# Kernel optimization log

Hardware: AMD Instinct MI355X
Metric: run time of the kernel (lower is better)

Reference implementation:

```python
import jax, jax.numpy as jnp
import numpy as np

E = 1024      # emb_size
H = 16        # num_heads
DH = E // H   # per-head dim (attn_output_emb_size)
DFF = 4096    # d_ff
LE = 4        # num_encoders
LD = 4        # num_decoders
B = 4
S_SRC = 512
S_TGT = 512
EPS = 1e-5
SCALE = float(np.sqrt(DH))


def _layernorm(x, g, b):
    m = jnp.mean(x, axis=-1, keepdims=True)
    v = jnp.mean((x - m) ** 2, axis=-1, keepdims=True)
    return (x - m) / jnp.sqrt(v + EPS) * g + b


def _mha(xq, xk, xv, wqkv, wo, bo, mask):
    # xq: [B,Sq,E]; wqkv: [3,H,E,DH]; mask: [B,Sq,St] or [B,1,St] with 0 / -inf entries.
    # Fuses the per-head SingleHeadSelfAttention loop into batched einsums; the
    # torch.cat(heads, dim=-1) order equals transpose(b,s,h,d)->reshape(b,s,E).
    Bn, Sq, En = xq.shape
    q = jnp.einsum('bse,hed->bhsd', xq, wqkv[0])
    k = jnp.einsum('bte,hed->bhtd', xk, wqkv[1])
    v = jnp.einsum('bte,hed->bhtd', xv, wqkv[2])
    scores = jnp.einsum('bhsd,bhtd->bhst', q, k) / SCALE
    # masked_fill(mask == -inf, -inf)
    scores = jnp.where(jnp.isneginf(mask)[:, None, :, :], -jnp.inf, scores)
    w = jax.nn.softmax(scores, axis=-1)
    o = jnp.einsum('bhst,bhtd->bhsd', w, v)
    o = o.transpose(0, 2, 1, 3).reshape(Bn, Sq, En)
    return o @ wo + bo


def _ffn(x, w1, b1, w2, b2):
    return jax.nn.relu(x @ w1 + b1) @ w2 + b2


def _forward(src, tgt, src_mask, tgt_mask, src_pad, tgt_pad, ep, dp):
    x = src.transpose(1, 0, 2)  # [B,Ss,E] (module is seq-first, heads go batch-first)
    y = tgt.transpose(1, 0, 2)  # [B,St,E]
    enc_mask = src_mask[None] + src_pad[:, None, :]   # [B,Ss,Ss]
    self_mask = tgt_mask[None] + tgt_pad[:, None, :]  # [B,St,St]
    cross_mask = src_pad[:, None, :]                  # [B,1,Ss]
    (wqkv, wo, bo, w1, b1, w2, b2, lg, lb) = ep
    for i in range(LE):  # post-norm encoder blocks
        x = x + _mha(x, x, x, wqkv[i], wo[i], bo[i], enc_mask)
        x = _layernorm(x, lg[i, 0], lb[i, 0])
        x = x + _ffn(x, w1[i], b1[i], w2[i], b2[i])
        x = _layernorm(x, lg[i, 1], lb[i, 1])
    (sqkv, swo, sbo, cqkv, cwo, cbo, dw1, db1, dw2, db2, dlg, dlb) = dp
    for i in range(LD):  # post-norm decoder blocks
        y = y + _mha(y, y, y, sqkv[i], swo[i], sbo[i], self_mask)
        y = _layernorm(y, dlg[i, 0], dlb[i, 0])
        y = y + _mha(y, x, x, cqkv[i], cwo[i], cbo[i], cross_mask)
        y = _layernorm(y, dlg[i, 1], dlb[i, 1])
        y = y + _ffn(y, dw1[i], db1[i], dw2[i], db2[i])
        y = _layernorm(y, dlg[i, 2], dlb[i, 2])
    return y.transpose(1, 0, 2)  # back to [St,B,E]


def setup_inputs() -> dict:
    key = jax.random.key(0)
    ks = iter(jax.random.split(key, 32))
    def p(shape):
        return jax.random.normal(next(ks), shape, jnp.float32) * 0.02
    # causal mask as produced by generate_square_subsequent_mask (0 on/below diag, -inf above)
    causal = jnp.where(jnp.triu(jnp.ones((S_TGT, S_TGT), bool), 1), -jnp.inf, 0.0).astype(jnp.float32)
    return {
        'src': jax.random.normal(next(ks), (S_SRC, B, E), jnp.float32),
        'tgt': jax.random.normal(next(ks), (S_TGT, B, E), jnp.float32),
        'src_mask': jnp.zeros((S_SRC, S_SRC), jnp.float32),
        'tgt_mask': causal,
        'src_padding_mask': jnp.zeros((B, S_SRC), jnp.float32),
        'tgt_padding_mask': jnp.zeros((B, S_TGT), jnp.float32),
        'enc_wqkv': p((LE, 3, H, E, DH)), 'enc_wo': p((LE, E, E)), 'enc_bo': jnp.zeros((LE, E), jnp.float32),
        'enc_ff_w1': p((LE, E, DFF)), 'enc_ff_b1': jnp.zeros((LE, DFF), jnp.float32),
        'enc_ff_w2': p((LE, DFF, E)), 'enc_ff_b2': jnp.zeros((LE, E), jnp.float32),
        'enc_ln_g': jnp.ones((LE, 2, E), jnp.float32), 'enc_ln_b': jnp.zeros((LE, 2, E), jnp.float32),
        'dec_wqkv_self': p((LD, 3, H, E, DH)), 'dec_wo_self': p((LD, E, E)), 'dec_bo_self': jnp.zeros((LD, E), jnp.float32),
        'dec_wqkv_cross': p((LD, 3, H, E, DH)), 'dec_wo_cross': p((LD, E, E)), 'dec_bo_cross': jnp.zeros((LD, E), jnp.float32),
        'dec_ff_w1': p((LD, E, DFF)), 'dec_ff_b1': jnp.zeros((LD, DFF), jnp.float32),
        'dec_ff_w2': p((LD, DFF, E)), 'dec_ff_b2': jnp.zeros((LD, E), jnp.float32),
        'dec_ln_g': jnp.ones((LD, 3, E), jnp.float32), 'dec_ln_b': jnp.zeros((LD, 3, E), jnp.float32),
    }


def reference(src, tgt, src_mask, tgt_mask, src_padding_mask, tgt_padding_mask,
              enc_wqkv, enc_wo, enc_bo, enc_ff_w1, enc_ff_b1, enc_ff_w2, enc_ff_b2,
              enc_ln_g, enc_ln_b,
              dec_wqkv_self, dec_wo_self, dec_bo_self,
              dec_wqkv_cross, dec_wo_cross, dec_bo_cross,
              dec_ff_w1, dec_ff_b1, dec_ff_w2, dec_ff_b2, dec_ln_g, dec_ln_b):
    ep = (enc_wqkv, enc_wo, enc_bo, enc_ff_w1, enc_ff_b1, enc_ff_w2, enc_ff_b2, enc_ln_g, enc_ln_b)
    dp = (dec_wqkv_self, dec_wo_self, dec_bo_self, dec_wqkv_cross, dec_wo_cross, dec_bo_cross,
          dec_ff_w1, dec_ff_b1, dec_ff_w2, dec_ff_b2, dec_ln_g, dec_ln_b)
    return _forward(src, tgt, src_mask, tgt_mask, src_padding_mask, tgt_padding_mask, ep, dp)
```

## Files before the change

### kernel.cpp

```cpp
#include <hip/hip_runtime.h>
#include <hip/hip_bf16.h>

typedef __hip_bfloat16 bf16;
typedef unsigned short u16;
typedef u16 u16x4 __attribute__((ext_vector_type(4)));
typedef u16 u16x8 __attribute__((ext_vector_type(8)));
typedef __bf16 bf16x8 __attribute__((ext_vector_type(8)));
typedef float f32x4 __attribute__((ext_vector_type(4)));

#define E_DIM 1024
#define DFF_DIM 4096
#define B_SZ 4
#define S_LEN 512
#define NTOK 2048

__device__ __forceinline__ u16 f2bf(float f) {
    unsigned u = __float_as_uint(f);
    return (u16)((u + 0x7FFFu + ((u >> 16) & 1u)) >> 16);
}
__device__ __forceinline__ void gload_lds16(const u16* g, u16* l) {
    __builtin_amdgcn_global_load_lds(
        (const __attribute__((address_space(1))) unsigned int*)g,
        (__attribute__((address_space(3))) unsigned int*)l, 16, 0, 0);
}

__global__ __launch_bounds__(256) void transpose_in(const float* __restrict__ in,
                                                    float* __restrict__ out,
                                                    u16* __restrict__ outb) {
    size_t i = (size_t)blockIdx.x * 256 + threadIdx.x;
    int e = (int)(i & 1023);
    int sb = (int)(i >> 10);
    int b = sb & 3;
    int s = sb >> 2;
    float v = in[i];
    size_t o = ((size_t)((b << 9) + s) << 10) + e;
    out[o] = v;
    outb[o] = f2bf(v);
}

__global__ __launch_bounds__(256) void writeout(const float* __restrict__ y,
                                                float* __restrict__ out) {
    size_t i = (size_t)blockIdx.x * 256 + threadIdx.x;
    int e = (int)(i & 1023);
    int sb = (int)(i >> 10);
    int b = sb & 3;
    int s = sb >> 2;
    out[i] = y[((size_t)((b << 9) + s) << 10) + e];
}

template<bool QKV>
__global__ __launch_bounds__(256) void cvt_wt(const float* __restrict__ W,
                                              u16* __restrict__ Wt, int K, int N,
                                              size_t wls, size_t wtls) {
    const float* Wl = W + (size_t)blockIdx.z * wls;
    u16* Wtl = Wt + (size_t)blockIdx.z * wtls;
    __shared__ u16 ts[64][72];
    const int n0 = blockIdx.x * 64, k0 = blockIdx.y * 64;
    #pragma unroll
    for (int r = 0; r < 16; ++r) {
        int idx = threadIdx.x + r * 256;
        int k = idx >> 6, n = idx & 63;
        float v;
        if (QKV) v = Wl[(size_t)((n0 + n) >> 6) * ((size_t)K * 64) + (size_t)(k0 + k) * 64 + ((n0 + n) & 63)];
        else     v = Wl[(size_t)(k0 + k) * N + n0 + n];
        ts[n][k] = f2bf(v);
    }
    __syncthreads();
    #pragma unroll
    for (int r = 0; r < 2; ++r) {
        int idx = threadIdx.x + r * 256;
        int n = idx >> 3, c = idx & 7;
        u16x8 vv = *reinterpret_cast<const u16x8*>(&ts[n][c * 8]);
        *reinterpret_cast<u16x8*>(Wtl + (size_t)(n0 + n) * K + k0 + c * 8) = vv;
    }
}

template<int BM, int EPI, bool BATCH>
__global__ __launch_bounds__(256) void gemm_bt(
    const u16* __restrict__ A,
    const u16* __restrict__ Bt,
    const float* __restrict__ bias,
    const float* __restrict__ Res, int ldres,
    void* __restrict__ Cout, int ldc, int Kfull, int KS, int gx,
    u16* __restrict__ vtout, int vcol0,
    size_t bstr, size_t cstr, size_t vstr)
{
    constexpr int MR = BM / 32;
    constexpr int AOPS = BM / 16;
    constexpr int BOPS = 8;
    constexpr int OPW = AOPS / 4 + BOPS / 4;
    __shared__ u16 As[3][BM * 32];
    __shared__ u16 Bs[3][128 * 32];
    const int tid = threadIdx.x;
    const int l = tid & 63, w = tid >> 6;
    const int nwg = gridDim.x;
    const int lin = blockIdx.x;
    const int wg = (lin & 7) * (nwg >> 3) + (lin >> 3);
    const int m0 = (wg / gx) * BM, n0 = (wg % gx) * 128;
    const int z = blockIdx.z;
    const int mw = (w >> 1) * (BM / 2), nw = (w & 1) * 64;
    const int lr = l & 15, lg = l >> 4;
    const int srow = l >> 2;
    const int schunk = (((l & 3) ^ ((l >> 3) & 3))) * 8;
    const int rsw = (lr >> 1) & 3;

    const u16* bt = Bt;
    u16* vto = vtout;
    size_t coff = 0;
    int koff = z * KS;
    if constexpr (BATCH) {
        bt += (size_t)z * bstr;
        vto += (size_t)z * vstr;
        coff = (size_t)z * cstr;
        koff = 0;
    }

    f32x4 acc[MR][4];
    #pragma unroll
    for (int mi = 0; mi < MR; ++mi)
        #pragma unroll
        for (int ni = 0; ni < 4; ++ni) acc[mi][ni] = (f32x4)(0.0f);

    const u16* ap = A + (size_t)(m0 + srow) * Kfull + koff + schunk;
    const u16* bp = bt + (size_t)(n0 + srow) * Kfull + koff + schunk;
    const int nt = KS / 32;

    #pragma unroll
    for (int op = w; op < AOPS; op += 4) gload_lds16(ap + (size_t)op * 16 * Kfull, &As[0][op * 512]);
    #pragma unroll
    for (int op = w; op < BOPS; op += 4) gload_lds16(bp + (size_t)op * 16 * Kfull, &Bs[0][op * 512]);
    #pragma unroll
    for (int op = w; op < AOPS; op += 4) gload_lds16(ap + (size_t)op * 16 * Kfull + 32, &As[1][op * 512]);
    #pragma unroll
    for (int op = w; op < BOPS; op += 4) gload_lds16(bp + (size_t)op * 16 * Kfull + 32, &Bs[1][op * 512]);

    for (int k = 0; k < nt; ++k) {
        if (k + 2 < nt) {
            const int kk = (k + 2) * 32;
            const int buf = (k + 2) % 3;
            #pragma unroll
            for (int op = w; op < AOPS; op += 4) gload_lds16(ap + (size_t)op * 16 * Kfull + kk, &As[buf][op * 512]);
            #pragma unroll
            for (int op = w; op < BOPS; op += 4) gload_lds16(bp + (size_t)op * 16 * Kfull + kk, &Bs[buf][op * 512]);
            asm volatile("s_waitcnt vmcnt(%0)" :: "i"(2 * OPW) : "memory");
        } else if (k + 1 < nt) {
            asm volatile("s_waitcnt vmcnt(%0)" :: "i"(OPW) : "memory");
        } else {
            asm volatile("s_waitcnt vmcnt(0)" ::: "memory");
        }
        __builtin_amdgcn_s_barrier();

        const int buf = k % 3;
        u16x8 af[MR], bfr[4];
        #pragma unroll
        for (int mi = 0; mi < MR; ++mi)
            af[mi] = *reinterpret_cast<const u16x8*>(
                &As[buf][(mw + mi * 16 + lr) * 32 + ((lg ^ rsw) * 8)]);
        #pragma unroll
        for (int ni = 0; ni < 4; ++ni)
            bfr[ni] = *reinterpret_cast<const u16x8*>(
                &Bs[buf][(nw + ni * 16 + lr) * 32 + ((lg ^ rsw) * 8)]);
        #pragma unroll
        for (int mi = 0; mi < MR; ++mi)
            #pragma unroll
            for (int ni = 0; ni < 4; ++ni)
                acc[mi][ni] = __builtin_amdgcn_mfma_f32_16x16x32_bf16(
                    __builtin_bit_cast(bf16x8, af[mi]),
                    __builtin_bit_cast(bf16x8, bfr[ni]),
                    acc[mi][ni], 0, 0, 0);
        __builtin_amdgcn_s_barrier();
    }

    #pragma unroll
    for (int mi = 0; mi < MR; ++mi) {
        #pragma unroll
        for (int ni = 0; ni < 4; ++ni) {
            const int gc = n0 + nw + ni * 16 + lr;
            float bv = 0.0f;
            if constexpr (EPI == 1 || EPI == 2) bv = bias[gc];
            #pragma unroll
            for (int r = 0; r < 4; ++r) {
                const int gr = m0 + mw + mi * 16 + lg * 4 + r;
                float v = acc[mi][ni][r] + bv;
                if constexpr (EPI == 1) v = fmaxf(v, 0.0f);
                if constexpr (EPI == 2) {
                    ((float*)Cout)[(size_t)gr * ldc + gc] = v + Res[(size_t)gr * ldres + gc];
                } else if constexpr (EPI == 3) {
                    ((float*)Cout)[(size_t)z * NTOK * ldc + (size_t)gr * ldc + gc] = v;
                } else {
                    if (gc >= vcol0) {
                        int d = gc - vcol0, hh = d >> 6, dd = d & 63;
                        int bb = gr >> 9, tt = gr & 511;
                        vto[((size_t)((bb * 16 + hh) * 64 + dd)) * 512 + tt] = f2bf(v);
                    } else {
                        ((u16*)Cout + coff)[(size_t)gr * ldc + gc] = f2bf(v);
                    }
                }
            }
        }
    }
}

template<int NP>
__global__ __launch_bounds__(256) void ln_red(
    const float* __restrict__ part, const float* __restrict__ bias,
    float* __restrict__ X,
    const float* __restrict__ g, const float* __restrict__ bta,
    u16* __restrict__ outb) {
    __shared__ float wred[4];
    __shared__ float stat;
    const size_t row = blockIdx.x;
    const int tid = threadIdx.x;
    float4 v = reinterpret_cast<const float4*>(X + (row << 10))[tid];
    const float4 bb = reinterpret_cast<const float4*>(bias)[tid];
    v.x += bb.x; v.y += bb.y; v.z += bb.z; v.w += bb.w;
    #pragma unroll
    for (int s = 0; s < NP; ++s) {
        const float4 p = reinterpret_cast<const float4*>(part + ((size_t)s * NTOK + row) * 1024)[tid];
        v.x += p.x; v.y += p.y; v.z += p.z; v.w += p.w;
    }
    float sm = v.x + v.y + v.z + v.w;
    #pragma unroll
    for (int off = 32; off; off >>= 1) sm += __shfl_down(sm, off, 64);
    if ((tid & 63) == 0) wred[tid >> 6] = sm;
    __syncthreads();
    if (tid == 0) stat = (wred[0] + wred[1] + wred[2] + wred[3]) * (1.0f / 1024.0f);
    __syncthreads();
    float m = stat;
    float dx = v.x - m, dy = v.y - m, dz = v.z - m, dw = v.w - m;
    float s2 = dx * dx + dy * dy + dz * dz + dw * dw;
    #pragma unroll
    for (int off = 32; off; off >>= 1) s2 += __shfl_down(s2, off, 64);
    __syncthreads();
    if ((tid & 63) == 0) wred[tid >> 6] = s2;
    __syncthreads();
    if (tid == 0) stat = rsqrtf((wred[0] + wred[1] + wred[2] + wred[3]) * (1.0f / 1024.0f) + 1e-5f);
    __syncthreads();
    float r = stat;
    const float4 gv = reinterpret_cast<const float4*>(g)[tid];
    const float4 bv = reinterpret_cast<const float4*>(bta)[tid];
    float4 o;
    o.x = dx * r * gv.x + bv.x;
    o.y = dy * r * gv.y + bv.y;
    o.z = dz * r * gv.z + bv.z;
    o.w = dw * r * gv.w + bv.w;
    reinterpret_cast<float4*>(X + (row << 10))[tid] = o;
    u16x4 ob;
    ob.x = f2bf(o.x); ob.y = f2bf(o.y); ob.z = f2bf(o.z); ob.w = f2bf(o.w);
    *reinterpret_cast<u16x4*>(outb + (row << 10) + (tid << 2)) = ob;
}

__global__ __launch_bounds__(256) void ln_kernel(float* __restrict__ X,
        const float* __restrict__ g, const float* __restrict__ bta,
        u16* __restrict__ outb) {
    __shared__ float wred[4];
    __shared__ float stat;
    float* x = X + ((size_t)blockIdx.x << 10);
    const int tid = threadIdx.x;
    float4 v = reinterpret_cast<float4*>(x)[tid];
    float s = v.x + v.y + v.z + v.w;
    #pragma unroll
    for (int off = 32; off; off >>= 1) s += __shfl_down(s, off, 64);
    if ((tid & 63) == 0) wred[tid >> 6] = s;
    __syncthreads();
    if (tid == 0) stat = (wred[0] + wred[1] + wred[2] + wred[3]) * (1.0f / 1024.0f);
    __syncthreads();
    float m = stat;
    float dx = v.x - m, dy = v.y - m, dz = v.z - m, dw = v.w - m;
    float s2 = dx * dx + dy * dy + dz * dz + dw * dw;
    #pragma unroll
    for (int off = 32; off; off >>= 1) s2 += __shfl_down(s2, off, 64);
    __syncthreads();
    if ((tid & 63) == 0) wred[tid >> 6] = s2;
    __syncthreads();
    if (tid == 0) stat = rsqrtf((wred[0] + wred[1] + wred[2] + wred[3]) * (1.0f / 1024.0f) + 1e-5f);
    __syncthreads();
    float r = stat;
    const float4 gv = reinterpret_cast<const float4*>(g)[tid];
    const float4 bv = reinterpret_cast<const float4*>(bta)[tid];
    float4 o;
    o.x = dx * r * gv.x + bv.x;
    o.y = dy * r * gv.y + bv.y;
    o.z = dz * r * gv.z + bv.z;
    o.w = dw * r * gv.w + bv.w;
    reinterpret_cast<float4*>(x)[tid] = o;
    u16x4 ob;
    ob.x = f2bf(o.x); ob.y = f2bf(o.y); ob.z = f2bf(o.z); ob.w = f2bf(o.w);
    *reinterpret_cast<u16x4*>(outb + ((size_t)blockIdx.x << 10) + (tid << 2)) = ob;
}

template<bool CAUSAL>
__global__ __launch_bounds__(256) void attn_mfma(
    const u16* __restrict__ Qb, int ldq,
    const u16* __restrict__ Kb, int ldk,
    const u16* __restrict__ Vt, u16* __restrict__ Ob, float inv_scale)
{
    __shared__ u16 sP[16][520];
    __shared__ float sMax[4][16];
    __shared__ float sSum[4][16];
    const int qt = blockIdx.x, h = blockIdx.y, b = blockIdx.z;
    const int tid = threadIdx.x;
    const int l = tid & 63, w = tid >> 6;
    const int lr = l & 15, lg = l >> 4;
    const int q = lr;
    const int tmax = CAUSAL ? (qt + 1) * 16 : 512;
    const int KT = CAUSAL ? ((qt + 2) >> 1) : 16;
    const int KT32 = KT * 32;

    const u16* qbase = Qb + (size_t)(b * 512 + qt * 16 + lr) * ldq + h * 64 + lg * 8;
    u16x8 qf0 = *reinterpret_cast<const u16x8*>(qbase);
    u16x8 qf1 = *reinterpret_cast<const u16x8*>(qbase + 32);

    f32x4 sacc[8];
    __builtin_amdgcn_s_setprio(1);
    #pragma unroll
    for (int ni = 0; ni < 8; ++ni) {
        const int t0 = w * 128 + ni * 16;
        if (CAUSAL && t0 >= tmax) { sacc[ni] = (f32x4)(-3.0e38f); continue; }
        const u16* kbase = Kb + (size_t)(b * 512 + t0 + lr) * ldk + h * 64 + lg * 8;
        u16x8 kf0 = *reinterpret_cast<const u16x8*>(kbase);
        u16x8 kf1 = *reinterpret_cast<const u16x8*>(kbase + 32);
        f32x4 sa = (f32x4)(0.0f);
        sa = __builtin_amdgcn_mfma_f32_16x16x32_bf16(
            __builtin_bit_cast(bf16x8, kf0), __builtin_bit_cast(bf16x8, qf0), sa, 0, 0, 0);
        sa = __builtin_amdgcn_mfma_f32_16x16x32_bf16(
            __builtin_bit_cast(bf16x8, kf1), __builtin_bit_cast(bf16x8, qf1), sa, 0, 0, 0);
        sacc[ni] = sa;
    }
    __builtin_amdgcn_s_setprio(0);
    float mx = -3.0e38f;
    #pragma unroll
    for (int ni = 0; ni < 8; ++ni) {
        const int t0 = w * 128 + ni * 16;
        #pragma unroll
        for (int r = 0; r < 4; ++r) {
            const int t = t0 + lg * 4 + r;
            float v = sacc[ni][r] * inv_scale;
            if (CAUSAL && t > qt * 16 + q) v = -3.0e38f;
            sacc[ni][r] = v;
            mx = fmaxf(mx, v);
        }
    }
    mx = fmaxf(mx, __shfl_xor(mx, 16));
    mx = fmaxf(mx, __shfl_xor(mx, 32));
    if (lg == 0) sMax[w][lr] = mx;
    __syncthreads();
    mx = fmaxf(fmaxf(sMax[0][q], sMax[1][q]), fmaxf(sMax[2][q], sMax[3][q]));

    float sum = 0.0f;
    #pragma unroll
    for (int ni = 0; ni < 8; ++ni)
        #pragma unroll
        for (int r = 0; r < 4; ++r) {
            float x = sacc[ni][r] - mx;
            float p = (x < -80.0f) ? 0.0f : __expf(x);
            sacc[ni][r] = p;
            sum += p;
        }
    sum += __shfl_xor(sum, 16);
    sum += __shfl_xor(sum, 32);
    if (lg == 0) sSum[w][lr] = sum;
    __syncthreads();
    const float inv = 1.0f / (sSum[0][q] + sSum[1][q] + sSum[2][q] + sSum[3][q]);

    const int sw = (q & 7) << 3;
    #pragma unroll
    for (int ni = 0; ni < 8; ++ni) {
        const int t0 = w * 128 + ni * 16;
        if (CAUSAL && t0 >= KT32) break;
        const int tb = t0 + lg * 4;
        unsigned p01 = (unsigned)f2bf(sacc[ni][0] * inv) | ((unsigned)f2bf(sacc[ni][1] * inv) << 16);
        unsigned p23 = (unsigned)f2bf(sacc[ni][2] * inv) | ((unsigned)f2bf(sacc[ni][3] * inv) << 16);
        *reinterpret_cast<unsigned*>(&sP[q][tb ^ sw]) = p01;
        *reinterpret_cast<unsigned*>(&sP[q][(tb + 2) ^ sw]) = p23;
    }
    __syncthreads();

    const u16* vbase = Vt + ((size_t)((b * 16 + h) * 64 + w * 16 + lr)) * 512 + lg * 8;
    const int swr = (lr & 7) << 3;
    f32x4 oa = (f32x4)(0.0f);
    __builtin_amdgcn_s_setprio(1);
    #pragma unroll 4
    for (int kt = 0; kt < KT; ++kt) {
        u16x8 pf = *reinterpret_cast<const u16x8*>(&sP[lr][(kt * 32 + lg * 8) ^ swr]);
        u16x8 vf = *reinterpret_cast<const u16x8*>(vbase + kt * 32);
        oa = __builtin_amdgcn_mfma_f32_16x16x32_bf16(
            __builtin_bit_cast(bf16x8, pf), __builtin_bit_cast(bf16x8, vf), oa, 0, 0, 0);
    }
    __builtin_amdgcn_s_setprio(0);
    #pragma unroll
    for (int r = 0; r < 4; ++r)
        Ob[(size_t)(b * 512 + qt * 16 + lg * 4 + r) * 1024 + h * 64 + w * 16 + lr] = f2bf(oa[r]);
}

extern "C" void kernel_launch(void* const* d_in, const int* in_sizes, int n_in,
                              void* d_out, int out_size, void* d_ws, size_t ws_size,
                              hipStream_t stream) {
    const float* src      = (const float*)d_in[0];
    const float* tgt      = (const float*)d_in[1];
    const float* enc_wqkv = (const float*)d_in[6];
    const float* enc_wo   = (const float*)d_in[7];
    const float* enc_bo   = (const float*)d_in[8];
    const float* enc_w1   = (const float*)d_in[9];
    const float* enc_b1   = (const float*)d_in[10];
    const float* enc_w2   = (const float*)d_in[11];
    const float* enc_b2   = (const float*)d_in[12];
    const float* enc_lg   = (const float*)d_in[13];
    const float* enc_lb   = (const float*)d_in[14];
    const float* dq_s     = (const float*)d_in[15];
    const float* dwo_s    = (const float*)d_in[16];
    const float* dbo_s    = (const float*)d_in[17];
    const float* dq_c     = (const float*)d_in[18];
    const float* dwo_c    = (const float*)d_in[19];
    const float* dbo_c    = (const float*)d_in[20];
    const float* dw1      = (const float*)d_in[21];
    const float* db1      = (const float*)d_in[22];
    const float* dw2      = (const float*)d_in[23];
    const float* db2      = (const float*)d_in[24];
    const float* dlg      = (const float*)d_in[25];
    const float* dlb      = (const float*)d_in[26];

    float* xe = (float*)d_ws;
    float* y  = xe + (size_t)NTOK * E_DIM;
    u16* xeb  = (u16*)(y + (size_t)NTOK * E_DIM);
    u16* yb   = xeb  + (size_t)NTOK * E_DIM;
    u16* qkvb = yb   + (size_t)NTOK * E_DIM;
    u16* attb = qkvb + (size_t)NTOK * 3 * E_DIM;
    u16* ffhb = qkvb;
    u16* wtbase = attb + (size_t)NTOK * E_DIM;

    const size_t SZ_QKV = (size_t)3072 * 1024;
    const size_t SZ_E   = (size_t)1024 * 1024;
    const size_t SZ_FF  = (size_t)4096 * 1024;
    const size_t o_eqkv = 0;
    const size_t o_ewo  = o_eqkv + 4 * SZ_QKV;
    const size_t o_ew1  = o_ewo  + 4 * SZ_E;
    const size_t o_ew2  = o_ew1  + 4 * SZ_FF;
    const size_t o_dqs  = o_ew2  + 4 * SZ_FF;
    const size_t o_dwos = o_dqs  + 4 * SZ_QKV;
    const size_t o_dqc  = o_dwos + 4 * SZ_E;
    const size_t o_dwoc = o_dqc  + 4 * SZ_QKV;
    const size_t o_dw1  = o_dwoc + 4 * SZ_E;
    const size_t o_dw2  = o_dw1  + 4 * SZ_FF;
    const size_t o_vt   = o_dw2  + 4 * SZ_FF;
    const size_t o_part = o_vt   + 2 * SZ_E;
    const size_t o_ck   = o_part + 16 * SZ_E;
    const size_t o_cvt  = o_ck   + 8 * SZ_E;
    const size_t act_bytes = (size_t)40 * 1024 * 1024;
    const size_t need_big = act_bytes + (o_cvt + 8 * SZ_E) * 2;
    const bool big = ws_size >= need_big;

    u16* vt   = big ? (wtbase + o_vt) : (wtbase + SZ_FF);
    float* part = big ? (float*)(wtbase + o_part) : nullptr;
    u16* ckb  = big ? (wtbase + o_ck) : nullptr;
    u16* cvtb = big ? (wtbase + o_cvt) : nullptr;
    const int HUGE_COL = 1 << 30;

    const size_t WQKV_L = 3 * (size_t)16 * E_DIM * 64;
    const dim3 blk(256);
    const dim3 g_attn(S_LEN / 16, 16, B_SZ);

    transpose_in<<<(NTOK * E_DIM) / 256, blk, 0, stream>>>(src, xe, xeb);
    transpose_in<<<(NTOK * E_DIM) / 256, blk, 0, stream>>>(tgt, y, yb);

    if (big) {
        cvt_wt<true ><<<dim3(48, 16, 4), blk, 0, stream>>>(enc_wqkv, wtbase + o_eqkv, 1024, 3072, WQKV_L, SZ_QKV);
        cvt_wt<false><<<dim3(16, 16, 4), blk, 0, stream>>>(enc_wo,   wtbase + o_ewo,  1024, 1024, SZ_E, SZ_E);
        cvt_wt<false><<<dim3(64, 16, 4), blk, 0, stream>>>(enc_w1,   wtbase + o_ew1,  1024, 4096, SZ_FF, SZ_FF);
        cvt_wt<false><<<dim3(16, 64, 4), blk, 0, stream>>>(enc_w2,   wtbase + o_ew2,  4096, 1024, SZ_FF, SZ_FF);
        cvt_wt<true ><<<dim3(48, 16, 4), blk, 0, stream>>>(dq_s,     wtbase + o_dqs,  1024, 3072, WQKV_L, SZ_QKV);
        cvt_wt<false><<<dim3(16, 16, 4), blk, 0, stream>>>(dwo_s,    wtbase + o_dwos, 1024, 1024, SZ_E, SZ_E);
        cvt_wt<true ><<<dim3(48, 16, 4), blk, 0, stream>>>(dq_c,     wtbase + o_dqc,  1024, 3072, WQKV_L, SZ_QKV);
        cvt_wt<false><<<dim3(16, 16, 4), blk, 0, stream>>>(dwo_c,    wtbase + o_dwoc, 1024, 1024, SZ_E, SZ_E);
        cvt_wt<false><<<dim3(64, 16, 4), blk, 0, stream>>>(dw1,      wtbase + o_dw1,  1024, 4096, SZ_FF, SZ_FF);
        cvt_wt<false><<<dim3(16, 64, 4), blk, 0, stream>>>(dw2,      wtbase + o_dw2,  4096, 1024, SZ_FF, SZ_FF);
    }

    for (int i = 0; i < 4; ++i) {
        u16* p_qkv = big ? wtbase + o_eqkv + i * SZ_QKV : wtbase;
        u16* p_wo  = big ? wtbase + o_ewo  + i * SZ_E   : wtbase;
        u16* p_w1  = big ? wtbase + o_ew1  + i * SZ_FF  : wtbase;
        u16* p_w2  = big ? wtbase + o_ew2  + i * SZ_FF  : wtbase;
        const float* lg0 = enc_lg + (size_t)(i * 2 + 0) * E_DIM;
        const float* lb0 = enc_lb + (size_t)(i * 2 + 0) * E_DIM;
        const float* lg1 = enc_lg + (size_t)(i * 2 + 1) * E_DIM;
        const float* lb1 = enc_lb + (size_t)(i * 2 + 1) * E_DIM;

        if (!big) cvt_wt<true><<<dim3(48, 16, 1), blk, 0, stream>>>(enc_wqkv + i * WQKV_L, p_qkv, 1024, 3072, 0, 0);
        gemm_bt<128, 0, false><<<dim3(384, 1, 1), blk, 0, stream>>>(xeb, p_qkv, nullptr, nullptr, 0, qkvb, 3072, 1024, 1024, 24, vt, 2048, 0, 0, 0);
        attn_mfma<false><<<g_attn, blk, 0, stream>>>(qkvb, 3072, qkvb + 1024, 3072, vt, attb, 0.125f);
        if (!big) cvt_wt<false><<<dim3(16, 16, 1), blk, 0, stream>>>(enc_wo + (size_t)i * SZ_E, p_wo, 1024, 1024, 0, 0);
        if (big) {
            gemm_bt<64, 3, false><<<dim3(256, 1, 2), blk, 0, stream>>>(attb, p_wo, nullptr, nullptr, 0, part, 1024, 1024, 512, 8, nullptr, HUGE_COL, 0, 0, 0);
            ln_red<2><<<NTOK, blk, 0, stream>>>(part, enc_bo + i * E_DIM, xe, lg0, lb0, xeb);
        } else {
            gemm_bt<64, 2, false><<<dim3(256, 1, 1), blk, 0, stream>>>(attb, p_wo, enc_bo + i * E_DIM, xe, 1024, xe, 1024, 1024, 1024, 8, nullptr, HUGE_COL, 0, 0, 0);
            ln_kernel<<<NTOK, blk, 0, stream>>>(xe, lg0, lb0, xeb);
        }
        if (!big) cvt_wt<false><<<dim3(64, 16, 1), blk, 0, stream>>>(enc_w1 + (size_t)i * SZ_FF, p_w1, 1024, 4096, 0, 0);
        gemm_bt<128, 1, false><<<dim3(512, 1, 1), blk, 0, stream>>>(xeb, p_w1, enc_b1 + i * DFF_DIM, nullptr, 0, ffhb, 4096, 1024, 1024, 32, nullptr, HUGE_COL, 0, 0, 0);
        if (!big) cvt_wt<false><<<dim3(16, 64, 1), blk, 0, stream>>>(enc_w2 + (size_t)i * SZ_FF, p_w2, 4096, 1024, 0, 0);
        if (big) {
            gemm_bt<128, 3, false><<<dim3(128, 1, 4), blk, 0, stream>>>(ffhb, p_w2, nullptr, nullptr, 0, part, 1024, 4096, 1024, 8, nullptr, HUGE_COL, 0, 0, 0);
            ln_red<4><<<NTOK, blk, 0, stream>>>(part, enc_b2 + i * E_DIM, xe, lg1, lb1, xeb);
        } else {
            gemm_bt<64, 2, false><<<dim3(256, 1, 1), blk, 0, stream>>>(ffhb, p_w2, enc_b2 + i * E_DIM, xe, 1024, xe, 1024, 4096, 4096, 8, nullptr, HUGE_COL, 0, 0, 0);
            ln_kernel<<<NTOK, blk, 0, stream>>>(xe, lg1, lb1, xeb);
        }
    }

    if (big) {
        gemm_bt<128, 0, true><<<dim3(256, 1, 4), blk, 0, stream>>>(
            xeb, wtbase + o_dqc + SZ_E, nullptr, nullptr, 0,
            ckb, 1024, 1024, 1024, 16, cvtb, 1024,
            SZ_QKV, 2 * SZ_E, 2 * SZ_E);
    }

    for (int i = 0; i < 4; ++i) {
        u16* p_qkv = big ? wtbase + o_dqs  + i * SZ_QKV : wtbase;
        u16* p_wos = big ? wtbase + o_dwos + i * SZ_E   : wtbase;
        u16* p_qc  = big ? wtbase + o_dqc  + i * SZ_QKV : wtbase;
        u16* p_woc = big ? wtbase + o_dwoc + i * SZ_E   : wtbase;
        u16* p_w1  = big ? wtbase + o_dw1  + i * SZ_FF  : wtbase;
        u16* p_w2  = big ? wtbase + o_dw2  + i * SZ_FF  : wtbase;
        const float* lg0 = dlg + (size_t)(i * 3 + 0) * E_DIM;
        const float* lb0 = dlb + (size_t)(i * 3 + 0) * E_DIM;
        const float* lg1 = dlg + (size_t)(i * 3 + 1) * E_DIM;
        const float* lb1 = dlb + (size_t)(i * 3 + 1) * E_DIM;
        const float* lg2 = dlg + (size_t)(i * 3 + 2) * E_DIM;
        const float* lb2 = dlb + (size_t)(i * 3 + 2) * E_DIM;

        if (!big) cvt_wt<true><<<dim3(48, 16, 1), blk, 0, stream>>>(dq_s + i * WQKV_L, p_qkv, 1024, 3072, 0, 0);
        gemm_bt<128, 0, false><<<dim3(384, 1, 1), blk, 0, stream>>>(yb, p_qkv, nullptr, nullptr, 0, qkvb, 3072, 1024, 1024, 24, vt, 2048, 0, 0, 0);
        attn_mfma<true><<<g_attn, blk, 0, stream>>>(qkvb, 3072, qkvb + 1024, 3072, vt, attb, 0.125f);
        if (!big) cvt_wt<false><<<dim3(16, 16, 1), blk, 0, stream>>>(dwo_s + (size_t)i * SZ_E, p_wos, 1024, 1024, 0, 0);
        if (big) {
            gemm_bt<64, 3, false><<<dim3(256, 1, 2), blk, 0, stream>>>(attb, p_wos, nullptr, nullptr, 0, part, 1024, 1024, 512, 8, nullptr, HUGE_COL, 0, 0, 0);
            ln_red<2><<<NTOK, blk, 0, stream>>>(part, dbo_s + i * E_DIM, y, lg0, lb0, yb);
        } else {
            gemm_bt<64, 2, false><<<dim3(256, 1, 1), blk, 0, stream>>>(attb, p_wos, dbo_s + i * E_DIM, y, 1024, y, 1024, 1024, 1024, 8, nullptr, HUGE_COL, 0, 0, 0);
            ln_kernel<<<NTOK, blk, 0, stream>>>(y, lg0, lb0, yb);
        }
        if (!big) cvt_wt<true><<<dim3(48, 16, 1), blk, 0, stream>>>(dq_c + i * WQKV_L, p_qc, 1024, 3072, 0, 0);
        gemm_bt<64, 0, false><<<dim3(256, 1, 1), blk, 0, stream>>>(yb, p_qc, nullptr, nullptr, 0, qkvb, 3072, 1024, 1024, 8, nullptr, HUGE_COL, 0, 0, 0);
        if (big) {
            attn_mfma<false><<<g_attn, blk, 0, stream>>>(qkvb, 3072, ckb + (size_t)i * 2 * SZ_E, 1024,
                                                         cvtb + (size_t)i * 2 * SZ_E, attb, 0.125f);
        } else {
            gemm_bt<64, 0, false><<<dim3(512, 1, 1), blk, 0, stream>>>(xeb, p_qc + SZ_E, nullptr, nullptr, 0, qkvb + 1024, 3072, 1024, 1024, 16, vt, 1024, 0, 0, 0);
            attn_mfma<false><<<g_attn, blk, 0, stream>>>(qkvb, 3072, qkvb + 1024, 3072, vt, attb, 0.125f);
        }
        if (!big) cvt_wt<false><<<dim3(16, 16, 1), blk, 0, stream>>>(dwo_c + (size_t)i * SZ_E, p_woc, 1024, 1024, 0, 0);
        if (big) {
            gemm_bt<64, 3, false><<<dim3(256, 1, 2), blk, 0, stream>>>(attb, p_woc, nullptr, nullptr, 0, part, 1024, 1024, 512, 8, nullptr, HUGE_COL, 0, 0, 0);
            ln_red<2><<<NTOK, blk, 0, stream>>>(part, dbo_c + i * E_DIM, y, lg1, lb1, yb);
        } else {
            gemm_bt<64, 2, false><<<dim3(256, 1, 1), blk, 0, stream>>>(attb, p_woc, dbo_c + i * E_DIM, y, 1024, y, 1024, 1024, 1024, 8, nullptr, HUGE_COL, 0, 0, 0);
            ln_kernel<<<NTOK, blk, 0, stream>>>(y, lg1, lb1, yb);
        }
        if (!big) cvt_wt<false><<<dim3(64, 16, 1), blk, 0, stream>>>(dw1 + (size_t)i * SZ_FF, p_w1, 1024, 4096, 0, 0);
        gemm_bt<128, 1, false><<<dim3(512, 1, 1), blk, 0, stream>>>(yb, p_w1, db1 + i * DFF_DIM, nullptr, 0, ffhb, 4096, 1024, 1024, 32, nullptr, HUGE_COL, 0, 0, 0);
        if (!big) cvt_wt<false><<<dim3(16, 64, 1), blk, 0, stream>>>(dw2 + (size_t)i * SZ_FF, p_w2, 4096, 1024, 0, 0);
        if (big) {
            gemm_bt<128, 3, false><<<dim3(128, 1, 4), blk, 0, stream>>>(ffhb, p_w2, nullptr, nullptr, 0, part, 1024, 4096, 1024, 8, nullptr, HUGE_COL, 0, 0, 0);
            ln_red<4><<<NTOK, blk, 0, stream>>>(part, db2 + i * E_DIM, y, lg2, lb2, yb);
        } else {
            gemm_bt<64, 2, false><<<dim3(256, 1, 1), blk, 0, stream>>>(ffhb, p_w2, db2 + i * E_DIM, y, 1024, y, 1024, 4096, 4096, 8, nullptr, HUGE_COL, 0, 0, 0);
            ln_kernel<<<NTOK, blk, 0, stream>>>(y, lg2, lb2, yb);
        }
    }

    writeout<<<(NTOK * E_DIM) / 256, blk, 0, stream>>>(y, (float*)d_out);
}
```

Measured before the change: 1.877 ms.

## Drop split-K partial-sum path and add column-major tile order for wide GEMMs

```diff
diff --git a/kernel.cpp b/kernel.cpp
--- a/kernel.cpp
+++ b/kernel.cpp
@@ -75,13 +75,13 @@
     }
 }
 
-template<int BM, int EPI, bool BATCH>
+template<int BM, int EPI, bool BATCH, bool CMAJ>
 __global__ __launch_bounds__(256) void gemm_bt(
     const u16* __restrict__ A,
     const u16* __restrict__ Bt,
     const float* __restrict__ bias,
     const float* __restrict__ Res, int ldres,
-    void* __restrict__ Cout, int ldc, int Kfull, int KS, int gx,
+    void* __restrict__ Cout, int ldc, int Kfull, int KS, int gdiv,
     u16* __restrict__ vtout, int vcol0,
     size_t bstr, size_t cstr, size_t vstr)
 {
@@ -96,7 +96,8 @@
     const int nwg = gridDim.x;
     const int lin = blockIdx.x;
     const int wg = (lin & 7) * (nwg >> 3) + (lin >> 3);
-    const int m0 = (wg / gx) * BM, n0 = (wg % gx) * 128;
+    const int m0 = (CMAJ ? (wg % gdiv) : (wg / gdiv)) * BM;
+    const int n0 = (CMAJ ? (wg / gdiv) : (wg % gdiv)) * 128;
     const int z = blockIdx.z;
     const int mw = (w >> 1) * (BM / 2), nw = (w & 1) * 64;
     const int lr = l & 15, lg = l >> 4;
@@ -185,8 +186,6 @@
                 if constexpr (EPI == 1) v = fmaxf(v, 0.0f);
                 if constexpr (EPI == 2) {
                     ((float*)Cout)[(size_t)gr * ldc + gc] = v + Res[(size_t)gr * ldres + gc];
-                } else if constexpr (EPI == 3) {
-                    ((float*)Cout)[(size_t)z * NTOK * ldc + (size_t)gr * ldc + gc] = v;
                 } else {
                     if (gc >= vcol0) {
                         int d = gc - vcol0, hh = d >> 6, dd = d & 63;
@@ -199,55 +198,6 @@
             }
         }
     }
-}
-
-template<int NP>
-__global__ __launch_bounds__(256) void ln_red(
-    const float* __restrict__ part, const float* __restrict__ bias,
-    float* __restrict__ X,
-    const float* __restrict__ g, const float* __restrict__ bta,
-    u16* __restrict__ outb) {
-    __shared__ float wred[4];
-    __shared__ float stat;
-    const size_t row = blockIdx.x;
-    const int tid = threadIdx.x;
-    float4 v = reinterpret_cast<const float4*>(X + (row << 10))[tid];
-    const float4 bb = reinterpret_cast<const float4*>(bias)[tid];
-    v.x += bb.x; v.y += bb.y; v.z += bb.z; v.w += bb.w;
-    #pragma unroll
-    for (int s = 0; s < NP; ++s) {
-        const float4 p = reinterpret_cast<const float4*>(part + ((size_t)s * NTOK + row) * 1024)[tid];
-        v.x += p.x; v.y += p.y; v.z += p.z; v.w += p.w;
-    }
-    float sm = v.x + v.y + v.z + v.w;
-    #pragma unroll
-    for (int off = 32; off; off >>= 1) sm += __shfl_down(sm, off, 64);
-    if ((tid & 63) == 0) wred[tid >> 6] = sm;
-    __syncthreads();
-    if (tid == 0) stat = (wred[0] + wred[1] + wred[2] + wred[3]) * (1.0f / 1024.0f);
-    __syncthreads();
-    float m = stat;
-    float dx = v.x - m, dy = v.y - m, dz = v.z - m, dw = v.w - m;
-    float s2 = dx * dx + dy * dy + dz * dz + dw * dw;
-    #pragma unroll
-    for (int off = 32; off; off >>= 1) s2 += __shfl_down(s2, off, 64);
-    __syncthreads();
-    if ((tid & 63) == 0) wred[tid >> 6] = s2;
-    __syncthreads();
-    if (tid == 0) stat = rsqrtf((wred[0] + wred[1] + wred[2] + wred[3]) * (1.0f / 1024.0f) + 1e-5f);
-    __syncthreads();
-    float r = stat;
-    const float4 gv = reinterpret_cast<const float4*>(g)[tid];
-    const float4 bv = reinterpret_cast<const float4*>(bta)[tid];
-    float4 o;
-    o.x = dx * r * gv.x + bv.x;
-    o.y = dy * r * gv.y + bv.y;
-    o.z = dz * r * gv.z + bv.z;
-    o.w = dw * r * gv.w + bv.w;
-    reinterpret_cast<float4*>(X + (row << 10))[tid] = o;
-    u16x4 ob;
-    ob.x = f2bf(o.x); ob.y = f2bf(o.y); ob.z = f2bf(o.z); ob.w = f2bf(o.w);
-    *reinterpret_cast<u16x4*>(outb + (row << 10) + (tid << 2)) = ob;
 }
 
 __global__ __launch_bounds__(256) void ln_kernel(float* __restrict__ X,
@@ -443,15 +393,13 @@
     const size_t o_dw1  = o_dwoc + 4 * SZ_E;
     const size_t o_dw2  = o_dw1  + 4 * SZ_FF;
     const size_t o_vt   = o_dw2  + 4 * SZ_FF;
-    const size_t o_part = o_vt   + 2 * SZ_E;
-    const size_t o_ck   = o_part + 16 * SZ_E;
+    const size_t o_ck   = o_vt   + 2 * SZ_E;
     const size_t o_cvt  = o_ck   + 8 * SZ_E;
     const size_t act_bytes = (size_t)40 * 1024 * 1024;
     const size_t need_big = act_bytes + (o_cvt + 8 * SZ_E) * 2;
     const bool big = ws_size >= need_big;
 
     u16* vt   = big ? (wtbase + o_vt) : (wtbase + SZ_FF);
-    float* part = big ? (float*)(wtbase + o_part) : nullptr;
     u16* ckb  = big ? (wtbase + o_ck) : nullptr;
     u16* cvtb = big ? (wtbase + o_cvt) : nullptr;
     const int HUGE_COL = 1 << 30;
@@ -487,30 +435,20 @@
         const float* lb1 = enc_lb + (size_t)(i * 2 + 1) * E_DIM;
 
         if (!big) cvt_wt<true><<<dim3(48, 16, 1), blk, 0, stream>>>(enc_wqkv + i * WQKV_L, p_qkv, 1024, 3072, 0, 0);
-        gemm_bt<128, 0, false><<<dim3(384, 1, 1), blk, 0, stream>>>(xeb, p_qkv, nullptr, nullptr, 0, qkvb, 3072, 1024, 1024, 24, vt, 2048, 0, 0, 0);
+        gemm_bt<128, 0, false, true><<<dim3(384, 1, 1), blk, 0, stream>>>(xeb, p_qkv, nullptr, nullptr, 0, qkvb, 3072, 1024, 1024, 16, vt, 2048, 0, 0, 0);
         attn_mfma<false><<<g_attn, blk, 0, stream>>>(qkvb, 3072, qkvb + 1024, 3072, vt, attb, 0.125f);
         if (!big) cvt_wt<false><<<dim3(16, 16, 1), blk, 0, stream>>>(enc_wo + (size_t)i * SZ_E, p_wo, 1024, 1024, 0, 0);
-        if (big) {
-            gemm_bt<64, 3, false><<<dim3(256, 1, 2), blk, 0, stream>>>(attb, p_wo, nullptr, nullptr, 0, part, 1024, 1024, 512, 8, nullptr, HUGE_COL, 0, 0, 0);
-            ln_red<2><<<NTOK, blk, 0, stream>>>(part, enc_bo + i * E_DIM, xe, lg0, lb0, xeb);
-        } else {
-            gemm_bt<64, 2, false><<<dim3(256, 1, 1), blk, 0, stream>>>(attb, p_wo, enc_bo + i * E_DIM, xe, 1024, xe, 1024, 1024, 1024, 8, nullptr, HUGE_COL, 0, 0, 0);
-            ln_kernel<<<NTOK, blk, 0, stream>>>(xe, lg0, lb0, xeb);
-        }
+        gemm_bt<64, 2, false, false><<<dim3(256, 1, 1), blk, 0, stream>>>(attb, p_wo, enc_bo + i * E_DIM, xe, 1024, xe, 1024, 1024, 1024, 8, nullptr, HUGE_COL, 0, 0, 0);
+        ln_kernel<<<NTOK, blk, 0, stream>>>(xe, lg0, lb0, xeb);
         if (!big) cvt_wt<false><<<dim3(64, 16, 1), blk, 0, stream>>>(enc_w1 + (size_t)i * SZ_FF, p_w1, 1024, 4096, 0, 0);
-        gemm_bt<128, 1, false><<<dim3(512, 1, 1), blk, 0, stream>>>(xeb, p_w1, enc_b1 + i * DFF_DIM, nullptr, 0, ffhb, 4096, 1024, 1024, 32, nullptr, HUGE_COL, 0, 0, 0);
+        gemm_bt<128, 1, false, true><<<dim3(512, 1, 1), blk, 0, stream>>>(xeb, p_w1, enc_b1 + i * DFF_DIM, nullptr, 0, ffhb, 4096, 1024, 1024, 16, nullptr, HUGE_COL, 0, 0, 0);
         if (!big) cvt_wt<false><<<dim3(16, 64, 1), blk, 0, stream>>>(enc_w2 + (size_t)i * SZ_FF, p_w2, 4096, 1024, 0, 0);
-        if (big) {
-            gemm_bt<128, 3, false><<<dim3(128, 1, 4), blk, 0, stream>>>(ffhb, p_w2, nullptr, nullptr, 0, part, 1024, 4096, 1024, 8, nullptr, HUGE_COL, 0, 0, 0);
-            ln_red<4><<<NTOK, blk, 0, stream>>>(part, enc_b2 + i * E_DIM, xe, lg1, lb1, xeb);
-        } else {
-            gemm_bt<64, 2, false><<<dim3(256, 1, 1), blk, 0, stream>>>(ffhb, p_w2, enc_b2 + i * E_DIM, xe, 1024, xe, 1024, 4096, 4096, 8, nullptr, HUGE_COL, 0, 0, 0);
-            ln_kernel<<<NTOK, blk, 0, stream>>>(xe, lg1, lb1, xeb);
-        }
+        gemm_bt<64, 2, false, false><<<dim3(256, 1, 1), blk, 0, stream>>>(ffhb, p_w2, enc_b2 + i * E_DIM, xe, 1024, xe, 1024, 4096, 4096, 8, nullptr, HUGE_COL, 0, 0, 0);
+        ln_kernel<<<NTOK, blk, 0, stream>>>(xe, lg1, lb1, xeb);
     }
 
     if (big) {
-        gemm_bt<128, 0, true><<<dim3(256, 1, 4), blk, 0, stream>>>(
+        gemm_bt<128, 0, true, true><<<dim3(256, 1, 4), blk, 0, stream>>>(
             xeb, wtbase + o_dqc + SZ_E, nullptr, nullptr, 0,
             ckb, 1024, 1024, 1024, 16, cvtb, 1024,
             SZ_QKV, 2 * SZ_E, 2 * SZ_E);
@@ -531,43 +469,28 @@
         const float* lb2 = dlb + (size_t)(i * 3 + 2) * E_DIM;
 
         if (!big) cvt_wt<true><<<dim3(48, 16, 1), blk, 0, stream>>>(dq_s + i * WQKV_L, p_qkv, 1024, 3072, 0, 0);
-        gemm_bt<128, 0, false><<<dim3(384, 1, 1), blk, 0, stream>>>(yb, p_qkv, nullptr, nullptr, 0, qkvb, 3072, 1024, 1024, 24, vt, 2048, 0, 0, 0);
+        gemm_bt<128, 0, false, true><<<dim3(384, 1, 1), blk, 0, stream>>>(yb, p_qkv, nullptr, nullptr, 0, qkvb, 3072, 1024, 1024, 16, vt, 2048, 0, 0, 0);
         attn_mfma<true><<<g_attn, blk, 0, stream>>>(qkvb, 3072, qkvb + 1024, 3072, vt, attb, 0.125f);
         if (!big) cvt_wt<false><<<dim3(16, 16, 1), blk, 0, stream>>>(dwo_s + (size_t)i * SZ_E, p_wos, 1024, 1024, 0, 0);
-        if (big) {
-            gemm_bt<64, 3, false><<<dim3(256, 1, 2), blk, 0, stream>>>(attb, p_wos, nullptr, nullptr, 0, part, 1024, 1024, 512, 8, nullptr, HUGE_COL, 0, 0, 0);
-            ln_red<2><<<NTOK, blk, 0, stream>>>(part, dbo_s + i * E_DIM, y, lg0, lb0, yb);
-        } else {
-            gemm_bt<64, 2, false><<<dim3(256, 1, 1), blk, 0, stream>>>(attb, p_wos, dbo_s + i * E_DIM, y, 1024, y, 1024, 1024, 1024, 8, nullptr, HUGE_COL, 0, 0, 0);
-            ln_kernel<<<NTOK, blk, 0, stream>>>(y, lg0, lb0, yb);
-        }
+        gemm_bt<64, 2, false, false><<<dim3(256, 1, 1), blk, 0, stream>>>(attb, p_wos, dbo_s + i * E_DIM, y, 1024, y, 1024, 1024, 1024, 8, nullptr, HUGE_COL, 0, 0, 0);
+        ln_kernel<<<NTOK, blk, 0, stream>>>(y, lg0, lb0, yb);
         if (!big) cvt_wt<true><<<dim3(48, 16, 1), blk, 0, stream>>>(dq_c + i * WQKV_L, p_qc, 1024, 3072, 0, 0);
-        gemm_bt<64, 0, false><<<dim3(256, 1, 1), blk, 0, stream>>>(yb, p_qc, nullptr, nullptr, 0, qkvb, 3072, 1024, 1024, 8, nullptr, HUGE_COL, 0, 0, 0);
+        gemm_bt<64, 0, false, false><<<dim3(256, 1, 1), blk, 0, stream>>>(yb, p_qc, nullptr, nullptr, 0, qkvb, 3072, 1024, 1024, 8, nullptr, HUGE_COL, 0, 0, 0);
         if (big) {
             attn_mfma<false><<<g_attn, blk, 0, stream>>>(qkvb, 3072, ckb + (size_t)i * 2 * SZ_E, 1024,
                                                          cvtb + (size_t)i * 2 * SZ_E, attb, 0.125f);
         } else {
-            gemm_bt<64, 0, false><<<dim3(512, 1, 1), blk, 0, stream>>>(xeb, p_qc + SZ_E, nullptr, nullptr, 0, qkvb + 1024, 3072, 1024, 1024, 16, vt, 1024, 0, 0, 0);
+            gemm_bt<64, 0, false, false><<<dim3(512, 1, 1), blk, 0, stream>>>(xeb, p_qc + SZ_E, nullptr, nullptr, 0, qkvb + 1024, 3072, 1024, 1024, 16, vt, 1024, 0, 0, 0);
             attn_mfma<false><<<g_attn, blk, 0, stream>>>(qkvb, 3072, qkvb + 1024, 3072, vt, attb, 0.125f);
         }
         if (!big) cvt_wt<false><<<dim3(16, 16, 1), blk, 0, stream>>>(dwo_c + (size_t)i * SZ_E, p_woc, 1024, 1024, 0, 0);
-        if (big) {
-            gemm_bt<64, 3, false><<<dim3(256, 1, 2), blk, 0, stream>>>(attb, p_woc, nullptr, nullptr, 0, part, 1024, 1024, 512, 8, nullptr, HUGE_COL, 0, 0, 0);
-            ln_red<2><<<NTOK, blk, 0, stream>>>(part, dbo_c + i * E_DIM, y, lg1, lb1, yb);
-        } else {
-            gemm_bt<64, 2, false><<<dim3(256, 1, 1), blk, 0, stream>>>(attb, p_woc, dbo_c + i * E_DIM, y, 1024, y, 1024, 1024, 1024, 8, nullptr, HUGE_COL, 0, 0, 0);
-            ln_kernel<<<NTOK, blk, 0, stream>>>(y, lg1, lb1, yb);
-        }
+        gemm_bt<64, 2, false, false><<<dim3(256, 1, 1), blk, 0, stream>>>(attb, p_woc, dbo_c + i * E_DIM, y, 1024, y, 1024, 1024, 1024, 8, nullptr, HUGE_COL, 0, 0, 0);
+        ln_kernel<<<NTOK, blk, 0, stream>>>(y, lg1, lb1, yb);
         if (!big) cvt_wt<false><<<dim3(64, 16, 1), blk, 0, stream>>>(dw1 + (size_t)i * SZ_FF, p_w1, 1024, 4096, 0, 0);
-        gemm_bt<128, 1, false><<<dim3(512, 1, 1), blk, 0, stream>>>(yb, p_w1, db1 + i * DFF_DIM, nullptr, 0, ffhb, 4096, 1024, 1024, 32, nullptr, HUGE_COL, 0, 0, 0);
+        gemm_bt<128, 1, false, true><<<dim3(512, 1, 1), blk, 0, stream>>>(yb, p_w1, db1 + i * DFF_DIM, nullptr, 0, ffhb, 4096, 1024, 1024, 16, nullptr, HUGE_COL, 0, 0, 0);
         if (!big) cvt_wt<false><<<dim3(16, 64, 1), blk, 0, stream>>>(dw2 + (size_t)i * SZ_FF, p_w2, 4096, 1024, 0, 0);
-        if (big) {
-            gemm_bt<128, 3, false><<<dim3(128, 1, 4), blk, 0, stream>>>(ffhb, p_w2, nullptr, nullptr, 0, part, 1024, 4096, 1024, 8, nullptr, HUGE_COL, 0, 0, 0);
-            ln_red<4><<<NTOK, blk, 0, stream>>>(part, db2 + i * E_DIM, y, lg2, lb2, yb);
-        } else {
-            gemm_bt<64, 2, false><<<dim3(256, 1, 1), blk, 0, stream>>>(ffhb, p_w2, db2 + i * E_DIM, y, 1024, y, 1024, 4096, 4096, 8, nullptr, HUGE_COL, 0, 0, 0);
-            ln_kernel<<<NTOK, blk, 0, stream>>>(y, lg2, lb2, yb);
-        }
+        gemm_bt<64, 2, false, false><<<dim3(256, 1, 1), blk, 0, stream>>>(ffhb, p_w2, db2 + i * E_DIM, y, 1024, y, 1024, 4096, 4096, 8, nullptr, HUGE_COL, 0, 0, 0);
+        ln_kernel<<<NTOK, blk, 0, stream>>>(y, lg2, lb2, yb);
     }
 
     writeout<<<(NTOK * E_DIM) / 256, blk, 0, stream>>>(y, (float*)d_out);
```

New measurement: 2.404 ms. +28.1%, slower.
